# Performance work log

Measured on AMD Instinct MI355X. Metric: run time of the kernel, lower is better.

The kernel has to match this reference:

```python
import jax, jax.numpy as jnp
import numpy as np

HEADS = 16


def setup_inputs() -> dict:
    key = jax.random.key(0)
    ks = jax.random.split(key, 6)
    B, S, D = 2, 2048, 1024
    return {
        "x": jax.random.normal(ks[0], (B, S, D), dtype=jnp.float32),
        "q_in": jax.random.normal(ks[1], (B, S, D), dtype=jnp.float32),
        "WQ": jax.random.normal(ks[2], (D, D), dtype=jnp.float32) * 0.03,
        "WK": jax.random.normal(ks[3], (D, D), dtype=jnp.float32) * 0.03,
        "WV": jax.random.normal(ks[4], (D, D), dtype=jnp.float32) * 0.03,
        "WO": jax.random.normal(ks[5], (D, D), dtype=jnp.float32) * 0.03,
    }


def reference(x, q_in, WQ, WK, WV, WO):
    B, S, D = x.shape
    H = HEADS
    hd = D // H
    # projections; tf.split on last dim == reshape to (B,S,H,hd)
    Q = (q_in @ WQ).reshape(B, S, H, hd)
    K = (x @ WK).reshape(B, S, H, hd)
    V = (x @ WV).reshape(B, S, H, hd)
    scores = jnp.einsum("bqhd,bkhd->bhqk", Q, K)  # [B,H,S,S]
    # causal additive mask: 0 on/below diagonal, -inf above
    causal = jnp.tril(jnp.ones((S, S), dtype=bool))
    mask = jnp.where(causal, 0.0, -jnp.inf).astype(scores.dtype)
    # NOTE: original adds the mask BEFORE scaling, and scales by sqrt(d_model)
    attn = jax.nn.softmax((scores + mask) / np.sqrt(D).astype(scores.dtype), axis=-1)
    ctx = jnp.einsum("bhqk,bkhd->bqhd", attn, V).reshape(B, S, D)
    return ctx @ WO
```

## Files before the change

### kernel.cpp

```cpp
#include <hip/hip_runtime.h>


typedef __bf16 bf16_t;
typedef __attribute__((ext_vector_type(8))) __bf16 bf16x8;
typedef __attribute__((ext_vector_type(4))) __bf16 bf16x4;
typedef __attribute__((ext_vector_type(4))) float f32x4;

#define SCALE_LOG2E 0.045084220027780106f
#define FIXED_MAX 8.0f

__device__ __forceinline__ void async_load16(const void* g, void* l) {
  __builtin_amdgcn_global_load_lds(
      (const __attribute__((address_space(1))) void*)g,
      (__attribute__((address_space(3))) void*)l, 16, 0, 0);
}

__global__ void cvt2(const float* __restrict__ x, const float* __restrict__ q,
                     bf16_t* __restrict__ xb, bf16_t* __restrict__ qb) {
  const size_t i = ((size_t)blockIdx.x * 256 + threadIdx.x) * 8;
  const float* src = blockIdx.y ? q : x;
  bf16_t* dst = blockIdx.y ? qb : xb;
  float4 v0 = *(const float4*)(src + i);
  float4 v1 = *(const float4*)(src + i + 4);
  bf16x8 o;
  o[0] = (bf16_t)v0.x; o[1] = (bf16_t)v0.y; o[2] = (bf16_t)v0.z; o[3] = (bf16_t)v0.w;
  o[4] = (bf16_t)v1.x; o[5] = (bf16_t)v1.y; o[6] = (bf16_t)v1.z; o[7] = (bf16_t)v1.w;
  *(bf16x8*)(dst + i) = o;
}

__global__ void cvtw(const float* __restrict__ w0, const float* __restrict__ w1,
                     const float* __restrict__ w2, const float* __restrict__ w3,
                     bf16_t* __restrict__ wt) {
  const float* W = blockIdx.z == 0 ? w0 : blockIdx.z == 1 ? w1 : blockIdx.z == 2 ? w2 : w3;
  bf16_t* dst = wt + (size_t)blockIdx.z * 1048576;
  const int c0 = blockIdx.x * 64, r0 = blockIdx.y * 64;
#pragma unroll
  for (int i = 0; i < 16; ++i) {
    int flat = i * 256 + threadIdx.x;
    int r = flat >> 6, c = flat & 63;
    dst[(size_t)(c0 + c) * 1024 + r0 + r] = (bf16_t)W[(size_t)(r0 + r) * 1024 + c0 + c];
  }
}

template <int MODE>
__global__ __launch_bounds__(256, MODE == 2 ? 4 : 2) void gemm128(
    const bf16_t* __restrict__ Aq, const bf16_t* __restrict__ Ax,
    const bf16_t* __restrict__ Bt,
    bf16_t* __restrict__ Cq, bf16_t* __restrict__ Cvt, float* __restrict__ Cf) {
  constexpr int K = 1024;
  constexpr int NT = (MODE == 2) ? 2 : 4;
  constexpr int NROWS = NT * 32;
  const int n0 = blockIdx.x * NROWS;
  const int m0 = blockIdx.y * 128;
  const bf16_t* A = (MODE == 0 && n0 >= 1024) ? Ax : Aq;

  __shared__ bf16_t lA[128 * 32];
  __shared__ bf16_t lB[NROWS * 32];

  const int tid = threadIdx.x;
  const int w = tid >> 6, l = tid & 63;
  const int wm = (w & 1) * 64, wn = (w >> 1) * (NT * 16);
  const int sr = l >> 2;
  const int sk = (l & 3) * 8;
  const int fr = l & 15, fc = (l >> 4) * 8;

  f32x4 acc[4][NT] = {};

  for (int kt = 0; kt < K; kt += 32) {
    __syncthreads();
#pragma unroll
    for (int c = 0; c < 2; ++c) {
      const int ch = w * 2 + c;
      async_load16(A + (size_t)(m0 + ch * 16 + sr) * K + kt + sk, &lA[ch * 512]);
      if (NT == 4 || c == 0) {
        const int bch = (NT == 4) ? ch : w;
        async_load16(Bt + (size_t)(n0 + bch * 16 + sr) * K + kt + sk, &lB[bch * 512]);
      }
    }
    __syncthreads();
    bf16x8 af[4], bfr[NT];
#pragma unroll
    for (int i = 0; i < 4; ++i) af[i] = *(const bf16x8*)&lA[(wm + i * 16 + fr) * 32 + fc];
#pragma unroll
    for (int j = 0; j < NT; ++j) bfr[j] = *(const bf16x8*)&lB[(wn + j * 16 + fr) * 32 + fc];
#pragma unroll
    for (int i = 0; i < 4; ++i)
#pragma unroll
      for (int j = 0; j < NT; ++j)
        acc[i][j] = __builtin_amdgcn_mfma_f32_16x16x32_bf16(af[i], bfr[j], acc[i][j], 0, 0, 0);
  }

  if (MODE == 2) {
#pragma unroll
    for (int i = 0; i < 4; ++i) {
      const int m = m0 + wm + i * 16 + (l >> 4) * 4;
#pragma unroll
      for (int j = 0; j < NT; ++j) {
        const int n = n0 + wn + j * 16 + fr;
#pragma unroll
        for (int r = 0; r < 4; ++r) Cf[(size_t)(m + r) * 1024 + n] = acc[i][j][r];
      }
    }
  } else if (n0 < 2048) {
#pragma unroll
    for (int i = 0; i < 4; ++i) {
      const int m = m0 + wm + i * 16 + (l >> 4) * 4;
#pragma unroll
      for (int j = 0; j < NT; ++j) {
        const int n = n0 + wn + j * 16 + fr;
#pragma unroll
        for (int r = 0; r < 4; ++r) Cq[(size_t)(m + r) * 3072 + n] = (bf16_t)acc[i][j][r];
      }
    }
  } else {
#pragma unroll
    for (int i = 0; i < 4; ++i) {
      const int mb = m0 + wm + i * 16 + (l >> 4) * 4;
      const int bb = mb >> 11, ss = mb & 2047;
#pragma unroll
      for (int j = 0; j < NT; ++j) {
        const int nn = n0 - 2048 + wn + j * 16 + fr;
        const int hh = nn >> 6, dd = nn & 63;
        bf16x4 pk;
#pragma unroll
        for (int r = 0; r < 4; ++r) pk[r] = (bf16_t)acc[i][j][r];
        *(bf16x4*)(Cvt + (size_t)((bb * 16 + hh) * 64 + dd) * 2048 + ss) = pk;
      }
    }
  }
}

__global__ __launch_bounds__(256, 2) void attn128(const bf16_t* __restrict__ qkv,
                                                  const bf16_t* __restrict__ vt,
                                                  bf16_t* __restrict__ ctx) {
  const int qt = 15 - blockIdx.y;
  const int bh = blockIdx.x;
  const int b = bh >> 4, h = bh & 15;
  const int tid = threadIdx.x, w = tid >> 6, l = tid & 63;
  const int fr = l & 15, fq = l >> 4;

  __shared__ __align__(16) bf16_t lK[2][64 * 64];
  __shared__ __align__(16) bf16_t lV[2][64 * 64];
  __shared__ __align__(16) bf16_t lP[4][32 * 72];

  const int q0 = qt * 128 + w * 32;

  bf16x8 qf[2][2];
#pragma unroll
  for (int u = 0; u < 2; ++u)
#pragma unroll
    for (int ks = 0; ks < 2; ++ks)
      qf[u][ks] = *(const bf16x8*)(qkv + (size_t)(b * 2048 + q0 + u * 16 + fr) * 3072 +
                                   h * 64 + ks * 32 + fq * 8);

  f32x4 o[2][4] = {};
  float li[2] = {0.f, 0.f};

  const int srow = l >> 3;
  const int swz = ((l & 7) ^ srow) * 8;
  const int xr = fr & 7;

  const int ktmax = 2 * qt + 1;
  const bf16_t* kg = qkv + (size_t)b * 2048 * 3072 + 1024 + h * 64;
  const bf16_t* vg = vt + (size_t)(b * 16 + h) * 64 * 2048;

#pragma unroll
  for (int c = 0; c < 2; ++c) {
    const int row = w * 16 + c * 8 + srow;
    async_load16(kg + (size_t)row * 3072 + swz, &lK[0][(w * 16 + c * 8) * 64]);
    async_load16(vg + (size_t)row * 2048 + swz, &lV[0][(w * 16 + c * 8) * 64]);
  }

  for (int kt = 0; kt <= ktmax; ++kt) {
    const int buf = kt & 1;
    __syncthreads();
    if (kt < ktmax) {
#pragma unroll
      for (int c = 0; c < 2; ++c) {
        const int row = w * 16 + c * 8 + srow;
        async_load16(kg + (size_t)((kt + 1) * 64 + row) * 3072 + swz,
                     &lK[buf ^ 1][(w * 16 + c * 8) * 64]);
        async_load16(vg + (size_t)row * 2048 + (kt + 1) * 64 + swz,
                     &lV[buf ^ 1][(w * 16 + c * 8) * 64]);
      }
    }

    f32x4 s[2][4] = {};
#pragma unroll
    for (int t = 0; t < 4; ++t)
#pragma unroll
      for (int ks = 0; ks < 2; ++ks) {
        bf16x8 kf = *(const bf16x8*)&lK[buf][(t * 16 + fr) * 64 + ((ks * 4 + fq) ^ xr) * 8];
        s[0][t] = __builtin_amdgcn_mfma_f32_16x16x32_bf16(kf, qf[0][ks], s[0][t], 0, 0, 0);
        s[1][t] = __builtin_amdgcn_mfma_f32_16x16x32_bf16(kf, qf[1][ks], s[1][t], 0, 0, 0);
      }

    const int kbase = kt * 64;
#pragma unroll
    for (int u = 0; u < 2; ++u) {
      const int qq = q0 + u * 16 + fr;
      const bool needmask = (kbase + 63) > (q0 + u * 16);
      float p[16];
#pragma unroll
      for (int t = 0; t < 4; ++t)
#pragma unroll
        for (int r = 0; r < 4; ++r) {
          float v = fmaf(s[u][t][r], SCALE_LOG2E, -FIXED_MAX);
          if (needmask && (kbase + t * 16 + fq * 4 + r > qq)) v = -1e30f;
          p[t * 4 + r] = __builtin_amdgcn_exp2f(v);
        }
      li[u] += ((((p[0] + p[1]) + (p[2] + p[3])) + ((p[4] + p[5]) + (p[6] + p[7]))) +
                (((p[8] + p[9]) + (p[10] + p[11])) + ((p[12] + p[13]) + (p[14] + p[15]))));
#pragma unroll
      for (int t = 0; t < 4; ++t) {
        bf16x4 pk;
        pk[0] = (bf16_t)p[t * 4 + 0]; pk[1] = (bf16_t)p[t * 4 + 1];
        pk[2] = (bf16_t)p[t * 4 + 2]; pk[3] = (bf16_t)p[t * 4 + 3];
        *(bf16x4*)&lP[w][(u * 16 + fr) * 72 + t * 16 + fq * 4] = pk;
      }
    }

    bf16x8 pf[2][2];
#pragma unroll
    for (int u = 0; u < 2; ++u)
#pragma unroll
      for (int g = 0; g < 2; ++g)
        pf[u][g] = *(const bf16x8*)&lP[w][(u * 16 + fr) * 72 + g * 32 + fq * 8];
#pragma unroll
    for (int g = 0; g < 2; ++g)
#pragma unroll
      for (int dt = 0; dt < 4; ++dt) {
        bf16x8 vf = *(const bf16x8*)&lV[buf][(dt * 16 + fr) * 64 + ((g * 4 + fq) ^ xr) * 8];
        o[0][dt] = __builtin_amdgcn_mfma_f32_16x16x32_bf16(vf, pf[0][g], o[0][dt], 0, 0, 0);
        o[1][dt] = __builtin_amdgcn_mfma_f32_16x16x32_bf16(vf, pf[1][g], o[1][dt], 0, 0, 0);
      }
  }

#pragma unroll
  for (int u = 0; u < 2; ++u) {
    float lsum = li[u];
    lsum += __shfl_xor(lsum, 16, 64);
    lsum += __shfl_xor(lsum, 32, 64);
    const float inv = 1.f / lsum;
    bf16_t* cb = ctx + (size_t)(b * 2048 + q0 + u * 16 + fr) * 1024 + h * 64;
#pragma unroll
    for (int dt = 0; dt < 4; ++dt) {
      bf16x4 ov;
#pragma unroll
      for (int r = 0; r < 4; ++r) ov[r] = (bf16_t)(o[u][dt][r] * inv);
      *(bf16x4*)(cb + dt * 16 + fq * 4) = ov;
    }
  }
}

extern "C" void kernel_launch(void* const* d_in, const int* in_sizes, int n_in,
                              void* d_out, int out_size, void* d_ws, size_t ws_size,
                              hipStream_t stream) {
  const float* x  = (const float*)d_in[0];
  const float* q  = (const float*)d_in[1];
  const float* WQ = (const float*)d_in[2];
  const float* WK = (const float*)d_in[3];
  const float* WV = (const float*)d_in[4];
  const float* WO = (const float*)d_in[5];
  float* out = (float*)d_out;

  bf16_t* qb  = (bf16_t*)d_ws;
  bf16_t* xb  = qb + 4194304;
  bf16_t* wt  = xb + 4194304;
  bf16_t* qkv = wt + 4194304;
  bf16_t* vtp = qkv + (size_t)4096 * 3072;
  bf16_t* ctx = vtp + 4194304;

  cvt2<<<dim3(2048, 2), 256, 0, stream>>>(x, q, xb, qb);
  cvtw<<<dim3(16, 16, 4), 256, 0, stream>>>(WQ, WK, WV, WO, wt);
  gemm128<0><<<dim3(24, 32), 256, 0, stream>>>(qb, xb, wt, qkv, vtp, nullptr);
  attn128<<<dim3(32, 16), 256, 0, stream>>>(qkv, vtp, ctx);
  gemm128<2><<<dim3(16, 32), 256, 0, stream>>>(ctx, ctx, wt + (size_t)3072 * 1024,
                                               nullptr, nullptr, out);
}
```

Before: 225.8 us.

## Merge conversion kernels, LDS-transpose weights, and trim attention work

```diff
diff --git a/kernel.cpp b/kernel.cpp
--- a/kernel.cpp
+++ b/kernel.cpp
@@ -15,30 +15,42 @@
       (__attribute__((address_space(3))) void*)l, 16, 0, 0);
 }
 
-__global__ void cvt2(const float* __restrict__ x, const float* __restrict__ q,
-                     bf16_t* __restrict__ xb, bf16_t* __restrict__ qb) {
-  const size_t i = ((size_t)blockIdx.x * 256 + threadIdx.x) * 8;
-  const float* src = blockIdx.y ? q : x;
-  bf16_t* dst = blockIdx.y ? qb : xb;
-  float4 v0 = *(const float4*)(src + i);
-  float4 v1 = *(const float4*)(src + i + 4);
-  bf16x8 o;
-  o[0] = (bf16_t)v0.x; o[1] = (bf16_t)v0.y; o[2] = (bf16_t)v0.z; o[3] = (bf16_t)v0.w;
-  o[4] = (bf16_t)v1.x; o[5] = (bf16_t)v1.y; o[6] = (bf16_t)v1.z; o[7] = (bf16_t)v1.w;
-  *(bf16x8*)(dst + i) = o;
-}
-
-__global__ void cvtw(const float* __restrict__ w0, const float* __restrict__ w1,
+__global__ void prep(const float* __restrict__ x, const float* __restrict__ q,
+                     const float* __restrict__ w0, const float* __restrict__ w1,
                      const float* __restrict__ w2, const float* __restrict__ w3,
+                     bf16_t* __restrict__ xb, bf16_t* __restrict__ qb,
                      bf16_t* __restrict__ wt) {
-  const float* W = blockIdx.z == 0 ? w0 : blockIdx.z == 1 ? w1 : blockIdx.z == 2 ? w2 : w3;
-  bf16_t* dst = wt + (size_t)blockIdx.z * 1048576;
-  const int c0 = blockIdx.x * 64, r0 = blockIdx.y * 64;
-#pragma unroll
-  for (int i = 0; i < 16; ++i) {
-    int flat = i * 256 + threadIdx.x;
-    int r = flat >> 6, c = flat & 63;
-    dst[(size_t)(c0 + c) * 1024 + r0 + r] = (bf16_t)W[(size_t)(r0 + r) * 1024 + c0 + c];
+  const int bid = blockIdx.x;
+  if (bid < 4096) {
+    const float* src = (bid >= 2048) ? q : x;
+    bf16_t* dst = (bid >= 2048) ? qb : xb;
+    const size_t i = ((size_t)(bid & 2047) * 256 + threadIdx.x) * 8;
+    float4 v0 = *(const float4*)(src + i);
+    float4 v1 = *(const float4*)(src + i + 4);
+    bf16x8 o;
+    o[0] = (bf16_t)v0.x; o[1] = (bf16_t)v0.y; o[2] = (bf16_t)v0.z; o[3] = (bf16_t)v0.w;
+    o[4] = (bf16_t)v1.x; o[5] = (bf16_t)v1.y; o[6] = (bf16_t)v1.z; o[7] = (bf16_t)v1.w;
+    *(bf16x8*)(dst + i) = o;
+  } else {
+    const int wb = bid - 4096;
+    const int z = wb >> 8;
+    const float* W = z == 0 ? w0 : z == 1 ? w1 : z == 2 ? w2 : w3;
+    bf16_t* dst = wt + (size_t)z * 1048576;
+    const int r0 = ((wb >> 4) & 15) * 64, c0 = (wb & 15) * 64;
+    __shared__ bf16_t t[64][72];
+#pragma unroll
+    for (int i = 0; i < 16; ++i) {
+      int flat = i * 256 + threadIdx.x;
+      int r = flat >> 6, c = flat & 63;
+      t[c][r] = (bf16_t)W[(size_t)(r0 + r) * 1024 + c0 + c];
+    }
+    __syncthreads();
+    const int c = threadIdx.x >> 2, seg = (threadIdx.x & 3) * 16;
+    bf16x8 a = *(const bf16x8*)&t[c][seg];
+    bf16x8 b = *(const bf16x8*)&t[c][seg + 8];
+    bf16_t* drow = dst + (size_t)(c0 + c) * 1024 + r0 + seg;
+    *(bf16x8*)drow = a;
+    *(bf16x8*)(drow + 8) = b;
   }
 }
 
@@ -133,7 +145,8 @@
 __global__ __launch_bounds__(256, 2) void attn128(const bf16_t* __restrict__ qkv,
                                                   const bf16_t* __restrict__ vt,
                                                   bf16_t* __restrict__ ctx) {
-  const int qt = 15 - blockIdx.y;
+  const int y = blockIdx.y;
+  const int qt = (y < 8) ? (15 - y) : (y - 8);
   const int bh = blockIdx.x;
   const int b = bh >> 4, h = bh & 15;
   const int tid = threadIdx.x, w = tid >> 6, l = tid & 63;
@@ -153,8 +166,12 @@
       qf[u][ks] = *(const bf16x8*)(qkv + (size_t)(b * 2048 + q0 + u * 16 + fr) * 3072 +
                                    h * 64 + ks * 32 + fq * 8);
 
+  bf16x8 ones;
+#pragma unroll
+  for (int i = 0; i < 8; ++i) ones[i] = (bf16_t)1.0f;
+
   f32x4 o[2][4] = {};
-  float li[2] = {0.f, 0.f};
+  f32x4 liacc[2] = {};
 
   const int srow = l >> 3;
   const int swz = ((l & 7) ^ srow) * 8;
@@ -185,6 +202,9 @@
       }
     }
 
+    const int kbase = kt * 64;
+    if (kbase > q0 + 31) continue;
+
     f32x4 s[2][4] = {};
 #pragma unroll
     for (int t = 0; t < 4; ++t)
@@ -195,27 +215,19 @@
         s[1][t] = __builtin_amdgcn_mfma_f32_16x16x32_bf16(kf, qf[1][ks], s[1][t], 0, 0, 0);
       }
 
-    const int kbase = kt * 64;
 #pragma unroll
     for (int u = 0; u < 2; ++u) {
       const int qq = q0 + u * 16 + fr;
       const bool needmask = (kbase + 63) > (q0 + u * 16);
-      float p[16];
-#pragma unroll
-      for (int t = 0; t < 4; ++t)
+#pragma unroll
+      for (int t = 0; t < 4; ++t) {
+        bf16x4 pk;
 #pragma unroll
         for (int r = 0; r < 4; ++r) {
           float v = fmaf(s[u][t][r], SCALE_LOG2E, -FIXED_MAX);
           if (needmask && (kbase + t * 16 + fq * 4 + r > qq)) v = -1e30f;
-          p[t * 4 + r] = __builtin_amdgcn_exp2f(v);
+          pk[r] = (bf16_t)__builtin_amdgcn_exp2f(v);
         }
-      li[u] += ((((p[0] + p[1]) + (p[2] + p[3])) + ((p[4] + p[5]) + (p[6] + p[7]))) +
-                (((p[8] + p[9]) + (p[10] + p[11])) + ((p[12] + p[13]) + (p[14] + p[15]))));
-#pragma unroll
-      for (int t = 0; t < 4; ++t) {
-        bf16x4 pk;
-        pk[0] = (bf16_t)p[t * 4 + 0]; pk[1] = (bf16_t)p[t * 4 + 1];
-        pk[2] = (bf16_t)p[t * 4 + 2]; pk[3] = (bf16_t)p[t * 4 + 3];
         *(bf16x4*)&lP[w][(u * 16 + fr) * 72 + t * 16 + fq * 4] = pk;
       }
     }
@@ -227,21 +239,21 @@
       for (int g = 0; g < 2; ++g)
         pf[u][g] = *(const bf16x8*)&lP[w][(u * 16 + fr) * 72 + g * 32 + fq * 8];
 #pragma unroll
-    for (int g = 0; g < 2; ++g)
+    for (int g = 0; g < 2; ++g) {
 #pragma unroll
       for (int dt = 0; dt < 4; ++dt) {
         bf16x8 vf = *(const bf16x8*)&lV[buf][(dt * 16 + fr) * 64 + ((g * 4 + fq) ^ xr) * 8];
         o[0][dt] = __builtin_amdgcn_mfma_f32_16x16x32_bf16(vf, pf[0][g], o[0][dt], 0, 0, 0);
         o[1][dt] = __builtin_amdgcn_mfma_f32_16x16x32_bf16(vf, pf[1][g], o[1][dt], 0, 0, 0);
       }
+      liacc[0] = __builtin_amdgcn_mfma_f32_16x16x32_bf16(ones, pf[0][g], liacc[0], 0, 0, 0);
+      liacc[1] = __builtin_amdgcn_mfma_f32_16x16x32_bf16(ones, pf[1][g], liacc[1], 0, 0, 0);
+    }
   }
 
 #pragma unroll
   for (int u = 0; u < 2; ++u) {
-    float lsum = li[u];
-    lsum += __shfl_xor(lsum, 16, 64);
-    lsum += __shfl_xor(lsum, 32, 64);
-    const float inv = 1.f / lsum;
+    const float inv = 1.f / liacc[u][0];
     bf16_t* cb = ctx + (size_t)(b * 2048 + q0 + u * 16 + fr) * 1024 + h * 64;
 #pragma unroll
     for (int dt = 0; dt < 4; ++dt) {
@@ -271,8 +283,7 @@
   bf16_t* vtp = qkv + (size_t)4096 * 3072;
   bf16_t* ctx = vtp + 4194304;
 
-  cvt2<<<dim3(2048, 2), 256, 0, stream>>>(x, q, xb, qb);
-  cvtw<<<dim3(16, 16, 4), 256, 0, stream>>>(WQ, WK, WV, WO, wt);
+  prep<<<dim3(5120), 256, 0, stream>>>(x, q, WQ, WK, WV, WO, xb, qb, wt);
   gemm128<0><<<dim3(24, 32), 256, 0, stream>>>(qb, xb, wt, qkv, vtp, nullptr);
   attn128<<<dim3(32, 16), 256, 0, stream>>>(qkv, vtp, ctx);
   gemm128<2><<<dim3(16, 32), 256, 0, stream>>>(ctx, ctx, wt + (size_t)3072 * 1024,
```

Result: faster. 200.6 us (-11.1%).
